# Kernel tuning notes

Hardware: AMD Instinct MI355X
Metric: run time of the kernel (lower is better)

Reference implementation:

```python
import jax, jax.numpy as jnp
import numpy as np

STRIDE, PAD, DIL, KH, KW = 1, 1, 1, 3, 3

def conv2d(x, w, b):
    y = jax.lax.conv_general_dilated(x, w, window_strides=(STRIDE, STRIDE),
                                     padding=((PAD, PAD), (PAD, PAD)),
                                     rhs_dilation=(DIL, DIL),
                                     dimension_numbers=('NCHW', 'OIHW', 'NCHW'))
    return y + b[None, :, None, None]

def deform_conv2d(x, offset, mask, weight):
    # x: [B,C,H,W]; offset: [B,2*KK,Ho,Wo] (y,x interleaved per kernel point);
    # mask: [B,KK,Ho,Wo]; weight: [O,C,KH,KW]
    B, C, H, W = x.shape
    O = weight.shape[0]
    KK = KH * KW
    Ho, Wo = offset.shape[2], offset.shape[3]
    off = offset.reshape(B, KK, 2, Ho, Wo)
    dy, dx = off[:, :, 0], off[:, :, 1]
    ki, kj = jnp.meshgrid(jnp.arange(KH), jnp.arange(KW), indexing='ij')
    ki = ki.reshape(KK).astype(x.dtype)
    kj = kj.reshape(KK).astype(x.dtype)
    base_y = (jnp.arange(Ho) * STRIDE - PAD).astype(x.dtype)
    base_x = (jnp.arange(Wo) * STRIDE - PAD).astype(x.dtype)
    yy = base_y[None, None, :, None] + ki[None, :, None, None] * DIL + dy  # [B,KK,Ho,Wo]
    xx = base_x[None, None, None, :] + kj[None, :, None, None] * DIL + dx

    def sample(img, ys, xs):  # img [C,H,W]; ys/xs [KK,Ho,Wo]
        y0f = jnp.floor(ys); x0f = jnp.floor(xs)
        wy = ys - y0f; wx = xs - x0f
        y0 = y0f.astype(jnp.int32); x0 = x0f.astype(jnp.int32)
        def gather(yi, xi):
            valid = (yi >= 0) & (yi < H) & (xi >= 0) & (xi < W)
            yc = jnp.clip(yi, 0, H - 1); xc = jnp.clip(xi, 0, W - 1)
            return img[:, yc, xc] * valid[None].astype(img.dtype)  # [C,KK,Ho,Wo]
        v00 = gather(y0, x0); v01 = gather(y0, x0 + 1)
        v10 = gather(y0 + 1, x0); v11 = gather(y0 + 1, x0 + 1)
        return (v00 * (1 - wy) * (1 - wx) + v01 * (1 - wy) * wx
                + v10 * wy * (1 - wx) + v11 * wy * wx)

    patches = jax.vmap(sample)(x, yy, xx)          # [B,C,KK,Ho,Wo]
    patches = patches * mask[:, None]              # modulation
    return jnp.einsum('bckhw,ock->bohw', patches, weight.reshape(O, C, KK))

def setup_inputs() -> dict:
    key = jax.random.key(0)
    ks = jax.random.split(key, 6)
    B, Cin, Cout, H, W = 8, 64, 64, 128, 128
    KK = KH * KW
    x = jax.random.normal(ks[0], (B, Cin, H, W), dtype=jnp.float32)
    # Note: original zero-inits offset/modulator convs; we use small random
    # weights so the deformable sampling path is nontrivially exercised.
    offset_w = jax.random.normal(ks[1], (2 * KK, Cin, KH, KW), dtype=jnp.float32) * 0.02
    offset_b = jax.random.normal(ks[2], (2 * KK,), dtype=jnp.float32) * 0.1
    mod_w = jax.random.normal(ks[3], (KK, Cin, KH, KW), dtype=jnp.float32) * 0.02
    mod_b = jax.random.normal(ks[4], (KK,), dtype=jnp.float32) * 0.1
    weight = jax.random.normal(ks[5], (Cout, Cin, KH, KW), dtype=jnp.float32) * (1.0 / np.sqrt(Cin * KK))
    return {"x": x, "offset_w": offset_w, "offset_b": offset_b,
            "mod_w": mod_w, "mod_b": mod_b, "weight": weight}

def reference(x, offset_w, offset_b, mod_w, mod_b, weight):
    offset = conv2d(x, offset_w, offset_b)                 # [B,2*KK,Ho,Wo]
    modulator = 2.0 * jax.nn.sigmoid(conv2d(x, mod_w, mod_b))  # [B,KK,Ho,Wo]
    return deform_conv2d(x, offset, modulator, weight)
```

## Files before the change

kernel.cpp:

```cpp
#include <hip/hip_runtime.h>
#include <math.h>

#define B_   8
#define C_   64
#define O_   64
#define H_   128
#define W_   128
#define HW_  (H_ * W_)
#define KSZ  576

typedef _Float16 f16x8 __attribute__((ext_vector_type(8)));
typedef float    f32x4 __attribute__((ext_vector_type(4)));

#define WPM_BYTES (18 * 4 * 64 * 8 * 2)
#define WPA_BYTES (18 * 2 * 64 * 8 * 2)
#define TB2_      (B_ * HW_ / 128)

__global__ __launch_bounds__(256) void prep_kernel(
    const float* __restrict__ x,
    const float* __restrict__ offw, const float* __restrict__ modw,
    const float* __restrict__ wgt,
    _Float16* __restrict__ xT, _Float16* __restrict__ wpM, _Float16* __restrict__ wpA)
{
    const int bi = blockIdx.x;
    if (bi < TB2_) {
        __shared__ _Float16 tile[128 * 68];
        const int tid = threadIdx.x;
        const int b      = bi >> 7;
        const int pxbase = (bi & 127) * 128;

        const int px4   = (tid & 31) * 4;
        const int cbase = tid >> 5;
        const float* __restrict__ xp = x + (size_t)b * C_ * HW_ + pxbase;
#pragma unroll
        for (int r = 0; r < 8; ++r) {
            const int c = cbase + r * 8;
            const f32x4 v = *(const f32x4*)&xp[(size_t)c * HW_ + px4];
#pragma unroll
            for (int i = 0; i < 4; ++i)
                tile[(px4 + i) * 68 + c] = (_Float16)v[i];
        }
        __syncthreads();

        const int px = tid >> 1;
        const int c0 = (tid & 1) * 32;
        f16x8 w[4];
#pragma unroll
        for (int q = 0; q < 4; ++q)
#pragma unroll
            for (int j = 0; j < 8; ++j)
                w[q][j] = tile[px * 68 + c0 + q * 8 + j];
        _Float16* __restrict__ op = xT + ((size_t)b * HW_ + pxbase + px) * 64 + c0;
#pragma unroll
        for (int q = 0; q < 4; ++q)
            *(f16x8*)&op[q * 8] = w[q];
        return;
    }
    const int g = (bi - TB2_) * 256 + threadIdx.x;
    if (g < 18 * 4 * 64) {
        const int s = g >> 8, mt = (g >> 6) & 3, lane = g & 63;
        const int k = s >> 1, cb = (s & 1) * 32;
        const int o  = mt * 16 + (lane & 15);
        const int c0 = cb + (lane >> 4) * 8;
        f16x8 v;
#pragma unroll
        for (int j = 0; j < 8; ++j) v[j] = (_Float16)wgt[o * KSZ + (c0 + j) * 9 + k];
        *(f16x8*)&wpM[(size_t)g * 8] = v;
    } else if (g < 18 * 4 * 64 + 18 * 2 * 64) {
        const int u = g - 18 * 4 * 64;
        const int s = u >> 7, mt = (u >> 6) & 1, lane = u & 63;
        const int k = s >> 1, cb = (s & 1) * 32;
        const int t  = mt * 16 + (lane & 15);
        const int c0 = cb + (lane >> 4) * 8;
        f16x8 v;
#pragma unroll
        for (int j = 0; j < 8; ++j) {
            float w = 0.0f;
            if (t < 18)      w = offw[t * KSZ + (c0 + j) * 9 + k];
            else if (t < 27) w = modw[(t - 18) * KSZ + (c0 + j) * 9 + k];
            v[j] = (_Float16)w;
        }
        *(f16x8*)&wpA[(size_t)u * 8] = v;
    }
}

__device__ __forceinline__ f16x8 splat8(_Float16 h) {
    f16x8 v = {h, h, h, h, h, h, h, h};
    return v;
}

#define WROWS 7
#define WCOLS 70

#define PP_IDX(t) (((t) & 3) | (((t) >> 4) << 2))
#define PP_SRC(t) ((((t) & 15) >> 2) * 16)

__global__ __launch_bounds__(256, 2) void dcn_main_kernel(
    const _Float16* __restrict__ xT,
    const _Float16* __restrict__ wpA,
    const _Float16* __restrict__ wpM,
    const float* __restrict__ offb,
    const float* __restrict__ modb,
    float* __restrict__ out)
{
    __shared__ _Float16 win[WROWS * WCOLS * 64];

    const int tid  = threadIdx.x;
    const int lane = tid & 63;
    const int wave = tid >> 6;
    const int lq   = lane >> 4;
    const int ln   = lane & 15;

    const int bi  = blockIdx.x;
    const int b   = bi & 7;
    const int r2  = bi >> 3;
    const int ho  = r2 >> 1;
    const int x0b = (r2 & 1) * 64;
    const int pxw = wave * 16 + ln;
    const int wo  = x0b + pxw;

    const _Float16* __restrict__ xbT = xT + (size_t)b * HW_ * 64;

#pragma unroll
    for (int it = 0; it < 16; ++it) {
        const int e = it * 256 + tid;
        if (e < WROWS * WCOLS * 8) {
            const int r   = e / (WCOLS * 8);
            const int rem = e - r * (WCOLS * 8);
            const int cx  = rem >> 3;
            const int q   = rem & 7;
            const int yr  = ho - 3 + r;
            const int xc  = x0b - 3 + cx;
            f16x8 v = splat8((_Float16)0.0f);
            if (((unsigned)yr < H_) && ((unsigned)xc < W_))
                v = *(const f16x8*)&xbT[((size_t)(yr * W_ + xc)) * 64 + q * 8];
            *(f16x8*)&win[(r * WCOLS + cx) * 64 + ((q ^ (cx & 7)) * 8)] = v;
        }
    }
    __syncthreads();

    f32x4 accA[2];
#pragma unroll
    for (int mt = 0; mt < 2; ++mt) accA[mt] = (f32x4){0.f, 0.f, 0.f, 0.f};

#pragma unroll
    for (int s = 0; s < 18; ++s) {
        const int k = s >> 1, h = s & 1;
        const int ki = k / 3, kj = k - ki * 3;
        f16x8 afA[2];
#pragma unroll
        for (int mt = 0; mt < 2; ++mt)
            afA[mt] = *(const f16x8*)&wpA[(size_t)((s * 2 + mt) * 64 + lane) * 8];
        const int sy = ki + 2;
        const int sx = pxw + kj + 2;
        const int chunk = h * 4 + lq;
        const f16x8 bfA = *(const f16x8*)&win[(sy * WCOLS + sx) * 64 + ((chunk ^ (sx & 7)) * 8)];
#pragma unroll
        for (int mt = 0; mt < 2; ++mt)
            accA[mt] = __builtin_amdgcn_mfma_f32_16x16x32_f16(afA[mt], bfA, accA[mt], 0, 0, 0);
    }

    float pp[8];
#pragma unroll
    for (int mt = 0; mt < 2; ++mt)
#pragma unroll
        for (int r = 0; r < 4; ++r) {
            const int t = mt * 16 + lq * 4 + r;
            const float val = accA[mt][r];
            float o = 0.0f;
            if (t < 18)      o = val + offb[t];
            else if (t < 27) o = 2.0f / (1.0f + expf(-(val + modb[t - 18])));
            pp[mt * 4 + r] = o;
        }

    float dyk[9], dxk[9], mkk[9];
#pragma unroll
    for (int k = 0; k < 9; ++k) {
        dyk[k] = __shfl(pp[PP_IDX(2 * k)],     PP_SRC(2 * k) + ln, 64);
        dxk[k] = __shfl(pp[PP_IDX(2 * k + 1)], PP_SRC(2 * k + 1) + ln, 64);
        mkk[k] = __shfl(pp[PP_IDX(18 + k)],    PP_SRC(18 + k) + ln, 64);
    }

    float w00k[9], w01k[9], w10k[9], w11k[9];
    int   b00k[9], b01k[9], b10k[9], b11k[9];
    int   ok00k[9], ok01k[9], ok10k[9], ok11k[9];
    int   y0k[9], x0k[9];
#pragma unroll
    for (int k = 0; k < 9; ++k) {
        const int ki = k / 3, kj = k - ki * 3;
        const float ys = (float)(ho - 1 + ki) + dyk[k];
        const float xs = (float)(wo - 1 + kj) + dxk[k];
        const float y0f = floorf(ys), x0f = floorf(xs);
        const float wy = ys - y0f, wx = xs - x0f;
        const int y0 = (int)y0f, x0 = (int)x0f;
        y0k[k] = y0; x0k[k] = x0;
        const float mk  = mkk[k];
        const float wyc = 1.0f - wy, wxc = 1.0f - wx;
        w00k[k] = wyc * wxc * mk;
        w01k[k] = wyc * wx  * mk;
        w10k[k] = wy  * wxc * mk;
        w11k[k] = wy  * wx  * mk;
        const int sy0 = y0 - ho + 3, sy1 = sy0 + 1;
        const int sx0 = x0 - x0b + 3, sx1 = sx0 + 1;
        const int oy0 = (unsigned)sy0 < WROWS, oy1 = (unsigned)sy1 < WROWS;
        const int ox0 = (unsigned)sx0 < WCOLS, ox1 = (unsigned)sx1 < WCOLS;
        ok00k[k] = oy0 & ox0; ok01k[k] = oy0 & ox1;
        ok10k[k] = oy1 & ox0; ok11k[k] = oy1 & ox1;
        const int r0 = sy0 * WCOLS, r1 = sy1 * WCOLS;
        const int e00 = (r0 + sx0) * 64 + ((lq ^ (sx0 & 7)) * 8);
        const int e01 = (r0 + sx1) * 64 + ((lq ^ (sx1 & 7)) * 8);
        const int e10 = (r1 + sx0) * 64 + ((lq ^ (sx0 & 7)) * 8);
        const int e11 = (r1 + sx1) * 64 + ((lq ^ (sx1 & 7)) * 8);
        b00k[k] = ok00k[k] ? e00 : 0;
        b01k[k] = ok01k[k] ? e01 : 0;
        b10k[k] = ok10k[k] ? e10 : 0;
        b11k[k] = ok11k[k] ? e11 : 0;
    }

    f32x4 acc[4];
#pragma unroll
    for (int mt = 0; mt < 4; ++mt) acc[mt] = (f32x4){0.f, 0.f, 0.f, 0.f};

#pragma unroll
    for (int k = 0; k < 9; ++k) {
        const f16x8 w00v = splat8((_Float16)w00k[k]);
        const f16x8 w01v = splat8((_Float16)w01k[k]);
        const f16x8 w10v = splat8((_Float16)w10k[k]);
        const f16x8 w11v = splat8((_Float16)w11k[k]);

#pragma unroll
        for (int h = 0; h < 2; ++h) {
            const int s  = 2 * k + h;
            const int hx = h << 5;
            const int c0 = h * 32 + lq * 8;

            f16x8 af[4];
#pragma unroll
            for (int mt = 0; mt < 4; ++mt)
                af[mt] = *(const f16x8*)&wpM[(size_t)((s * 4 + mt) * 64 + lane) * 8];

            f16x8 a00 = *(const f16x8*)&win[b00k[k] ^ hx];
            f16x8 a01 = *(const f16x8*)&win[b01k[k] ^ hx];
            f16x8 a10 = *(const f16x8*)&win[b10k[k] ^ hx];
            f16x8 a11 = *(const f16x8*)&win[b11k[k] ^ hx];

            if (__builtin_expect(!ok00k[k], 0)) {
                const int yc = min(max(y0k[k], 0), H_ - 1), xc = min(max(x0k[k], 0), W_ - 1);
                const bool in = ((unsigned)y0k[k] < H_) && ((unsigned)x0k[k] < W_);
                a00 = in ? *(const f16x8*)&xbT[((size_t)(yc * W_ + xc)) * 64 + c0] : splat8((_Float16)0.0f);
            }
            if (__builtin_expect(!ok01k[k], 0)) {
                const int yc = min(max(y0k[k], 0), H_ - 1), xc = min(max(x0k[k] + 1, 0), W_ - 1);
                const bool in = ((unsigned)y0k[k] < H_) && ((unsigned)(x0k[k] + 1) < W_);
                a01 = in ? *(const f16x8*)&xbT[((size_t)(yc * W_ + xc)) * 64 + c0] : splat8((_Float16)0.0f);
            }
            if (__builtin_expect(!ok10k[k], 0)) {
                const int yc = min(max(y0k[k] + 1, 0), H_ - 1), xc = min(max(x0k[k], 0), W_ - 1);
                const bool in = ((unsigned)(y0k[k] + 1) < H_) && ((unsigned)x0k[k] < W_);
                a10 = in ? *(const f16x8*)&xbT[((size_t)(yc * W_ + xc)) * 64 + c0] : splat8((_Float16)0.0f);
            }
            if (__builtin_expect(!ok11k[k], 0)) {
                const int yc = min(max(y0k[k] + 1, 0), H_ - 1), xc = min(max(x0k[k] + 1, 0), W_ - 1);
                const bool in = ((unsigned)(y0k[k] + 1) < H_) && ((unsigned)(x0k[k] + 1) < W_);
                a11 = in ? *(const f16x8*)&xbT[((size_t)(yc * W_ + xc)) * 64 + c0] : splat8((_Float16)0.0f);
            }

            f16x8 r = a00 * w00v;
            r = a01 * w01v + r;
            r = a10 * w10v + r;
            r = a11 * w11v + r;

#pragma unroll
            for (int mt = 0; mt < 4; ++mt)
                acc[mt] = __builtin_amdgcn_mfma_f32_16x16x32_f16(af[mt], r, acc[mt], 0, 0, 0);
        }
    }

    float* __restrict__ ob = out + (size_t)b * O_ * HW_ + (size_t)ho * W_;
#pragma unroll
    for (int mt = 0; mt < 4; ++mt)
#pragma unroll
        for (int r = 0; r < 4; ++r) {
            const int o = mt * 16 + lq * 4 + r;
            ob[(size_t)o * HW_ + wo] = acc[mt][r];
        }
}

extern "C" void kernel_launch(void* const* d_in, const int* in_sizes, int n_in,
                              void* d_out, int out_size, void* d_ws, size_t ws_size,
                              hipStream_t stream) {
    (void)in_sizes; (void)n_in; (void)out_size; (void)ws_size;
    const float* x    = (const float*)d_in[0];
    const float* offw = (const float*)d_in[1];
    const float* offb = (const float*)d_in[2];
    const float* modw = (const float*)d_in[3];
    const float* modb = (const float*)d_in[4];
    const float* wgt  = (const float*)d_in[5];
    float* out = (float*)d_out;

    _Float16* wpM = (_Float16*)d_ws;
    _Float16* wpA = (_Float16*)((char*)d_ws + WPM_BYTES);
    _Float16* xT  = (_Float16*)((char*)d_ws + WPM_BYTES + WPA_BYTES);

    prep_kernel<<<TB2_ + 27, 256, 0, stream>>>(x, offw, modw, wgt, xT, wpM, wpA);
    dcn_main_kernel<<<B_ * H_ * 2, 256, 0, stream>>>(xT, wpA, wpM, offb, modb, out);
}
```

Measured before the change: 149.6 us.

## Halve LDS window by staging channel halves and shrink offset-conv tile

The main kernel now loads only a 3x66 halo window for the offset/modulator convolution, then reuses shared memory to stage the 7x70 deformable window in two 32-channel halves, one per pass. The main loop is reordered to iterate channel-half outer and kernel point inner, and the out-of-window flags are packed into one bitmask. This halves LDS footprint to raise occupancy and cuts the initial load volume, at the cost of extra barriers and a second window load. The min-blocks launch bound is removed, which may change register allocation.

```diff
diff --git a/kernel.cpp b/kernel.cpp
--- a/kernel.cpp
+++ b/kernel.cpp
@@ -89,13 +89,15 @@
     return v;
 }
 
-#define WROWS 7
-#define WCOLS 70
+#define AROWS 3
+#define ACOLS 66
+#define BROWS 7
+#define BCOLS 70
 
 #define PP_IDX(t) (((t) & 3) | (((t) >> 4) << 2))
 #define PP_SRC(t) ((((t) & 15) >> 2) * 16)
 
-__global__ __launch_bounds__(256, 2) void dcn_main_kernel(
+__global__ __launch_bounds__(256) void dcn_main_kernel(
     const _Float16* __restrict__ xT,
     const _Float16* __restrict__ wpA,
     const _Float16* __restrict__ wpM,
@@ -103,7 +105,7 @@
     const float* __restrict__ modb,
     float* __restrict__ out)
 {
-    __shared__ _Float16 win[WROWS * WCOLS * 64];
+    __shared__ _Float16 win[BROWS * BCOLS * 32];
 
     const int tid  = threadIdx.x;
     const int lane = tid & 63;
@@ -122,19 +124,19 @@
     const _Float16* __restrict__ xbT = xT + (size_t)b * HW_ * 64;
 
 #pragma unroll
-    for (int it = 0; it < 16; ++it) {
+    for (int it = 0; it < 7; ++it) {
         const int e = it * 256 + tid;
-        if (e < WROWS * WCOLS * 8) {
-            const int r   = e / (WCOLS * 8);
-            const int rem = e - r * (WCOLS * 8);
+        if (e < AROWS * ACOLS * 8) {
+            const int r   = e / (ACOLS * 8);
+            const int rem = e - r * (ACOLS * 8);
             const int cx  = rem >> 3;
             const int q   = rem & 7;
-            const int yr  = ho - 3 + r;
-            const int xc  = x0b - 3 + cx;
+            const int yr  = ho - 1 + r;
+            const int xc  = x0b - 1 + cx;
             f16x8 v = splat8((_Float16)0.0f);
             if (((unsigned)yr < H_) && ((unsigned)xc < W_))
                 v = *(const f16x8*)&xbT[((size_t)(yr * W_ + xc)) * 64 + q * 8];
-            *(f16x8*)&win[(r * WCOLS + cx) * 64 + ((q ^ (cx & 7)) * 8)] = v;
+            *(f16x8*)&win[(r * ACOLS + cx) * 64 + ((q ^ (cx & 7)) * 8)] = v;
         }
     }
     __syncthreads();
@@ -151,10 +153,9 @@
 #pragma unroll
         for (int mt = 0; mt < 2; ++mt)
             afA[mt] = *(const f16x8*)&wpA[(size_t)((s * 2 + mt) * 64 + lane) * 8];
-        const int sy = ki + 2;
-        const int sx = pxw + kj + 2;
+        const int sx = pxw + kj;
         const int chunk = h * 4 + lq;
-        const f16x8 bfA = *(const f16x8*)&win[(sy * WCOLS + sx) * 64 + ((chunk ^ (sx & 7)) * 8)];
+        const f16x8 bfA = *(const f16x8*)&win[(ki * ACOLS + sx) * 64 + ((chunk ^ (sx & 7)) * 8)];
 #pragma unroll
         for (int mt = 0; mt < 2; ++mt)
             accA[mt] = __builtin_amdgcn_mfma_f32_16x16x32_f16(afA[mt], bfA, accA[mt], 0, 0, 0);
@@ -173,48 +174,44 @@
             pp[mt * 4 + r] = o;
         }
 
-    float dyk[9], dxk[9], mkk[9];
-#pragma unroll
-    for (int k = 0; k < 9; ++k) {
-        dyk[k] = __shfl(pp[PP_IDX(2 * k)],     PP_SRC(2 * k) + ln, 64);
-        dxk[k] = __shfl(pp[PP_IDX(2 * k + 1)], PP_SRC(2 * k + 1) + ln, 64);
-        mkk[k] = __shfl(pp[PP_IDX(18 + k)],    PP_SRC(18 + k) + ln, 64);
-    }
-
     float w00k[9], w01k[9], w10k[9], w11k[9];
     int   b00k[9], b01k[9], b10k[9], b11k[9];
-    int   ok00k[9], ok01k[9], ok10k[9], ok11k[9];
-    int   y0k[9], x0k[9];
+    int   oks[9];
+    int   y0s[9], x0s[9];
 #pragma unroll
     for (int k = 0; k < 9; ++k) {
         const int ki = k / 3, kj = k - ki * 3;
-        const float ys = (float)(ho - 1 + ki) + dyk[k];
-        const float xs = (float)(wo - 1 + kj) + dxk[k];
+        const float dy = __shfl(pp[PP_IDX(2 * k)],     PP_SRC(2 * k) + ln, 64);
+        const float dx = __shfl(pp[PP_IDX(2 * k + 1)], PP_SRC(2 * k + 1) + ln, 64);
+        const float mk = __shfl(pp[PP_IDX(18 + k)],    PP_SRC(18 + k) + ln, 64);
+
+        const float ys = (float)(ho - 1 + ki) + dy;
+        const float xs = (float)(wo - 1 + kj) + dx;
         const float y0f = floorf(ys), x0f = floorf(xs);
         const float wy = ys - y0f, wx = xs - x0f;
         const int y0 = (int)y0f, x0 = (int)x0f;
-        y0k[k] = y0; x0k[k] = x0;
-        const float mk  = mkk[k];
+        y0s[k] = y0; x0s[k] = x0;
         const float wyc = 1.0f - wy, wxc = 1.0f - wx;
         w00k[k] = wyc * wxc * mk;
         w01k[k] = wyc * wx  * mk;
         w10k[k] = wy  * wxc * mk;
         w11k[k] = wy  * wx  * mk;
+
         const int sy0 = y0 - ho + 3, sy1 = sy0 + 1;
         const int sx0 = x0 - x0b + 3, sx1 = sx0 + 1;
-        const int oy0 = (unsigned)sy0 < WROWS, oy1 = (unsigned)sy1 < WROWS;
-        const int ox0 = (unsigned)sx0 < WCOLS, ox1 = (unsigned)sx1 < WCOLS;
-        ok00k[k] = oy0 & ox0; ok01k[k] = oy0 & ox1;
-        ok10k[k] = oy1 & ox0; ok11k[k] = oy1 & ox1;
-        const int r0 = sy0 * WCOLS, r1 = sy1 * WCOLS;
-        const int e00 = (r0 + sx0) * 64 + ((lq ^ (sx0 & 7)) * 8);
-        const int e01 = (r0 + sx1) * 64 + ((lq ^ (sx1 & 7)) * 8);
-        const int e10 = (r1 + sx0) * 64 + ((lq ^ (sx0 & 7)) * 8);
-        const int e11 = (r1 + sx1) * 64 + ((lq ^ (sx1 & 7)) * 8);
-        b00k[k] = ok00k[k] ? e00 : 0;
-        b01k[k] = ok01k[k] ? e01 : 0;
-        b10k[k] = ok10k[k] ? e10 : 0;
-        b11k[k] = ok11k[k] ? e11 : 0;
+        const int oy0 = (unsigned)sy0 < BROWS, oy1 = (unsigned)sy1 < BROWS;
+        const int ox0 = (unsigned)sx0 < BCOLS, ox1 = (unsigned)sx1 < BCOLS;
+        const int ok00 = oy0 & ox0, ok01 = oy0 & ox1;
+        const int ok10 = oy1 & ox0, ok11 = oy1 & ox1;
+        oks[k] = ok00 | (ok01 << 1) | (ok10 << 2) | (ok11 << 3);
+        const int e00 = ((sy0 * BCOLS + sx0) * 32) + ((lq ^ (sx0 & 3)) * 8);
+        const int e01 = ((sy0 * BCOLS + sx1) * 32) + ((lq ^ (sx1 & 3)) * 8);
+        const int e10 = ((sy1 * BCOLS + sx0) * 32) + ((lq ^ (sx0 & 3)) * 8);
+        const int e11 = ((sy1 * BCOLS + sx1) * 32) + ((lq ^ (sx1 & 3)) * 8);
+        b00k[k] = ok00 ? e00 : 0;
+        b01k[k] = ok01 ? e01 : 0;
+        b10k[k] = ok10 ? e10 : 0;
+        b11k[k] = ok11 ? e11 : 0;
     }
 
     f32x4 acc[4];
@@ -222,53 +219,71 @@
     for (int mt = 0; mt < 4; ++mt) acc[mt] = (f32x4){0.f, 0.f, 0.f, 0.f};
 
 #pragma unroll
-    for (int k = 0; k < 9; ++k) {
-        const f16x8 w00v = splat8((_Float16)w00k[k]);
-        const f16x8 w01v = splat8((_Float16)w01k[k]);
-        const f16x8 w10v = splat8((_Float16)w10k[k]);
-        const f16x8 w11v = splat8((_Float16)w11k[k]);
-
-#pragma unroll
-        for (int h = 0; h < 2; ++h) {
-            const int s  = 2 * k + h;
-            const int hx = h << 5;
-            const int c0 = h * 32 + lq * 8;
+    for (int h = 0; h < 2; ++h) {
+        const int cb = h * 32;
+        __syncthreads();
+#pragma unroll
+        for (int it = 0; it < 8; ++it) {
+            const int e = it * 256 + tid;
+            if (e < BROWS * BCOLS * 4) {
+                const int r   = e / (BCOLS * 4);
+                const int rem = e - r * (BCOLS * 4);
+                const int cx  = rem >> 2;
+                const int q   = rem & 3;
+                const int yr  = ho - 3 + r;
+                const int xc  = x0b - 3 + cx;
+                f16x8 v = splat8((_Float16)0.0f);
+                if (((unsigned)yr < H_) && ((unsigned)xc < W_))
+                    v = *(const f16x8*)&xbT[((size_t)(yr * W_ + xc)) * 64 + cb + q * 8];
+                *(f16x8*)&win[(r * BCOLS + cx) * 32 + ((q ^ (cx & 3)) * 8)] = v;
+            }
+        }
+        __syncthreads();
+
+        const int c0 = cb + lq * 8;
+#pragma unroll
+        for (int k = 0; k < 9; ++k) {
+            const int s = 2 * k + h;
 
             f16x8 af[4];
 #pragma unroll
             for (int mt = 0; mt < 4; ++mt)
                 af[mt] = *(const f16x8*)&wpM[(size_t)((s * 4 + mt) * 64 + lane) * 8];
 
-            f16x8 a00 = *(const f16x8*)&win[b00k[k] ^ hx];
-            f16x8 a01 = *(const f16x8*)&win[b01k[k] ^ hx];
-            f16x8 a10 = *(const f16x8*)&win[b10k[k] ^ hx];
-            f16x8 a11 = *(const f16x8*)&win[b11k[k] ^ hx];
-
-            if (__builtin_expect(!ok00k[k], 0)) {
-                const int yc = min(max(y0k[k], 0), H_ - 1), xc = min(max(x0k[k], 0), W_ - 1);
-                const bool in = ((unsigned)y0k[k] < H_) && ((unsigned)x0k[k] < W_);
-                a00 = in ? *(const f16x8*)&xbT[((size_t)(yc * W_ + xc)) * 64 + c0] : splat8((_Float16)0.0f);
+            f16x8 a00 = *(const f16x8*)&win[b00k[k]];
+            f16x8 a01 = *(const f16x8*)&win[b01k[k]];
+            f16x8 a10 = *(const f16x8*)&win[b10k[k]];
+            f16x8 a11 = *(const f16x8*)&win[b11k[k]];
+
+            const int okk = oks[k];
+            if (__builtin_expect(okk != 15, 0)) {
+                const int y0 = y0s[k], x0 = x0s[k];
+                if (!(okk & 1)) {
+                    const int yc = min(max(y0, 0), H_ - 1), xc = min(max(x0, 0), W_ - 1);
+                    const bool in = ((unsigned)y0 < H_) && ((unsigned)x0 < W_);
+                    a00 = in ? *(const f16x8*)&xbT[((size_t)(yc * W_ + xc)) * 64 + c0] : splat8((_Float16)0.0f);
+                }
+                if (!(okk & 2)) {
+                    const int yc = min(max(y0, 0), H_ - 1), xc = min(max(x0 + 1, 0), W_ - 1);
+                    const bool in = ((unsigned)y0 < H_) && ((unsigned)(x0 + 1) < W_);
+                    a01 = in ? *(const f16x8*)&xbT[((size_t)(yc * W_ + xc)) * 64 + c0] : splat8((_Float16)0.0f);
+                }
+                if (!(okk & 4)) {
+                    const int yc = min(max(y0 + 1, 0), H_ - 1), xc = min(max(x0, 0), W_ - 1);
+                    const bool in = ((unsigned)(y0 + 1) < H_) && ((unsigned)x0 < W_);
+                    a10 = in ? *(const f16x8*)&xbT[((size_t)(yc * W_ + xc)) * 64 + c0] : splat8((_Float16)0.0f);
+                }
+                if (!(okk & 8)) {
+                    const int yc = min(max(y0 + 1, 0), H_ - 1), xc = min(max(x0 + 1, 0), W_ - 1);
+                    const bool in = ((unsigned)(y0 + 1) < H_) && ((unsigned)(x0 + 1) < W_);
+                    a11 = in ? *(const f16x8*)&xbT[((size_t)(yc * W_ + xc)) * 64 + c0] : splat8((_Float16)0.0f);
+                }
             }
-            if (__builtin_expect(!ok01k[k], 0)) {
-                const int yc = min(max(y0k[k], 0), H_ - 1), xc = min(max(x0k[k] + 1, 0), W_ - 1);
-                const bool in = ((unsigned)y0k[k] < H_) && ((unsigned)(x0k[k] + 1) < W_);
-                a01 = in ? *(const f16x8*)&xbT[((size_t)(yc * W_ + xc)) * 64 + c0] : splat8((_Float16)0.0f);
-            }
-            if (__builtin_expect(!ok10k[k], 0)) {
-                const int yc = min(max(y0k[k] + 1, 0), H_ - 1), xc = min(max(x0k[k], 0), W_ - 1);
-                const bool in = ((unsigned)(y0k[k] + 1) < H_) && ((unsigned)x0k[k] < W_);
-                a10 = in ? *(const f16x8*)&xbT[((size_t)(yc * W_ + xc)) * 64 + c0] : splat8((_Float16)0.0f);
-            }
-            if (__builtin_expect(!ok11k[k], 0)) {
-                const int yc = min(max(y0k[k] + 1, 0), H_ - 1), xc = min(max(x0k[k] + 1, 0), W_ - 1);
-                const bool in = ((unsigned)(y0k[k] + 1) < H_) && ((unsigned)(x0k[k] + 1) < W_);
-                a11 = in ? *(const f16x8*)&xbT[((size_t)(yc * W_ + xc)) * 64 + c0] : splat8((_Float16)0.0f);
-            }
-
-            f16x8 r = a00 * w00v;
-            r = a01 * w01v + r;
-            r = a10 * w10v + r;
-            r = a11 * w11v + r;
+
+            f16x8 r = a00 * splat8((_Float16)w00k[k]);
+            r = a01 * splat8((_Float16)w01k[k]) + r;
+            r = a10 * splat8((_Float16)w10k[k]) + r;
+            r = a11 * splat8((_Float16)w11k[k]) + r;
 
 #pragma unroll
             for (int mt = 0; mt < 4; ++mt)
```

Measured after the change: 155.3 us. +3.8%, slower.
